# Kernel tuning notes

Hardware: AMD Instinct MI355X
Metric: run time of the kernel (lower is better)

## Reference

```python
import jax, jax.numpy as jnp
import numpy as np

HID = 2048
NH = 16
HD = HID // NH
FF = 8192
SEQ = 2048
B = 1
EPS = 1e-05
ROPE_BASE = 10000.0


def _layernorm(x, w, b):
    mu = jnp.mean(x, axis=-1, keepdims=True)
    var = jnp.mean(jnp.square(x - mu), axis=-1, keepdims=True)
    return (x - mu) * jax.lax.rsqrt(var + EPS) * w + b


def _rope(x, offset):
    # x: [B, S, H, D]; rotate-half LLaMA-style rotary embedding
    S, D = x.shape[1], x.shape[3]
    inv_freq = 1.0 / (ROPE_BASE ** (jnp.arange(0, D, 2, dtype=jnp.float32) / D))  # [D/2]
    pos = jnp.arange(S, dtype=jnp.float32) + offset
    ang = pos[:, None] * inv_freq[None, :]                     # [S, D/2]
    cos = jnp.cos(ang)[None, :, None, :]                       # [1,S,1,D/2]
    sin = jnp.sin(ang)[None, :, None, :]
    x1, x2 = x[..., : D // 2], x[..., D // 2 :]
    return jnp.concatenate([x1 * cos - x2 * sin, x2 * cos + x1 * sin], axis=-1)


def setup_inputs() -> dict:
    key = jax.random.key(0)
    ks = jax.random.split(key, 16)
    sd = 0.02
    inp = {
        "hidden_states": jax.random.normal(ks[0], (B, SEQ, HID), dtype=jnp.float32),
        # additive causal mask as fed to multi_head_attention_forward
        "attention_mask": jnp.where(
            jnp.tril(jnp.ones((SEQ, SEQ), dtype=bool)), 0.0, -1e9
        ).astype(jnp.float32),
        "ln1_w": jnp.ones((HID,), jnp.float32),
        "ln1_b": jnp.zeros((HID,), jnp.float32),
        "ln2_w": jnp.ones((HID,), jnp.float32),
        "ln2_b": jnp.zeros((HID,), jnp.float32),
        "wq": jax.random.normal(ks[1], (HID, HID), jnp.float32) * sd,
        "bq": jnp.zeros((HID,), jnp.float32),
        "wk": jax.random.normal(ks[2], (HID, HID), jnp.float32) * sd,
        "bk": jnp.zeros((HID,), jnp.float32),
        "wv": jax.random.normal(ks[3], (HID, HID), jnp.float32) * sd,
        "bv": jnp.zeros((HID,), jnp.float32),
        "wo": jax.random.normal(ks[4], (HID, HID), jnp.float32) * sd,
        "bo": jnp.zeros((HID,), jnp.float32),
        "w_gate": jax.random.normal(ks[5], (FF, HID), jnp.float32) * sd,
        "w_up": jax.random.normal(ks[6], (FF, HID), jnp.float32) * sd,
        "w_down": jax.random.normal(ks[7], (HID, FF), jnp.float32) * sd,
        "total_seq_len": SEQ,
    }
    return inp


def reference(hidden_states, attention_mask, ln1_w, ln1_b, ln2_w, ln2_b,
              wq, bq, wk, bk, wv, bv, wo, bo, w_gate, w_up, w_down,
              total_seq_len):
    Bv, S, _ = hidden_states.shape
    x = _layernorm(hidden_states, ln1_w, ln1_b)
    q = (x @ wq.T + bq).reshape(Bv, S, NH, HD)
    k = (x @ wk.T + bk).reshape(Bv, S, NH, HD)
    v = (x @ wv.T + bv).reshape(Bv, S, NH, HD)
    offset = total_seq_len - S  # 0 for prefill
    q = _rope(q, offset)
    k = _rope(k, offset)
    # cache of max_sequence_length zeros concatenated with k/v then sliced to the
    # last total_seq_len entries == just the current k/v when total_seq_len == S
    scale = 1.0 / np.sqrt(HD)
    scores = jnp.einsum("bshd,bthd->bhst", q, k) * scale + attention_mask[None, None]
    probs = jax.nn.softmax(scores, axis=-1)
    attn = jnp.einsum("bhst,bthd->bshd", probs, v).reshape(Bv, S, HID)
    attn = attn @ wo.T + bo
    h = hidden_states + attn
    y = _layernorm(h, ln2_w, ln2_b)
    ffn = (jax.nn.silu(y @ w_gate.T) * (y @ w_up.T)) @ w_down.T
    return h + ffn
```

## Files before the change

kernel.cpp:

```cpp
#include <hip/hip_runtime.h>

#define HIDN 2048
#define NHEAD 16
#define HDIM 128
#define FFDIM 8192
#define SEQLEN 2048

typedef __attribute__((ext_vector_type(8))) __bf16 bf16x8;
typedef __attribute__((ext_vector_type(4))) float f32x4;
typedef __attribute__((ext_vector_type(4))) unsigned short u16x4;
typedef __attribute__((ext_vector_type(8))) unsigned short u16x8;

__device__ __forceinline__ unsigned short f2bfu(float f) {
    unsigned int u = __float_as_uint(f);
    unsigned int r = u + 0x7fffu + ((u >> 16) & 1u);
    return (unsigned short)(r >> 16);
}
__device__ __forceinline__ float bfu2f(unsigned short u) {
    return __uint_as_float(((unsigned int)u) << 16);
}

__device__ __forceinline__ void gload16(const void* g, void* l) {
    __builtin_amdgcn_global_load_lds(
        (const __attribute__((address_space(1))) unsigned int*)g,
        (__attribute__((address_space(3))) unsigned int*)l,
        16, 0, 0);
}

__device__ __forceinline__ void conv_groups(const float* __restrict__ src,
                                            unsigned short* __restrict__ dst,
                                            int i0, int stride, int n8) {
    for (int i = i0; i < n8; i += stride) {
        float4 a = ((const float4*)src)[i * 2];
        float4 b = ((const float4*)src)[i * 2 + 1];
        u16x8 v;
        v[0] = f2bfu(a.x); v[1] = f2bfu(a.y); v[2] = f2bfu(a.z); v[3] = f2bfu(a.w);
        v[4] = f2bfu(b.x); v[5] = f2bfu(b.y); v[6] = f2bfu(b.z); v[7] = f2bfu(b.w);
        *(u16x8*)(dst + (size_t)i * 8) = v;
    }
}

__global__ __launch_bounds__(256)
void conv_f32_bf16(const float* __restrict__ src, unsigned short* __restrict__ dst) {
    int i = blockIdx.x * 256 + threadIdx.x;
    conv_groups(src, dst, i, 1 << 30, i + 1);
}

__global__ __launch_bounds__(256)
void conv3_f32_bf16(const float* __restrict__ s0, const float* __restrict__ s1,
                    const float* __restrict__ s2, unsigned short* __restrict__ dst) {
    int i = blockIdx.x * 256 + threadIdx.x;
    int m = i >> 19;
    int li = i & ((1 << 19) - 1);
    const float* s = (m == 0) ? s0 : (m == 1) ? s1 : s2;
    float4 a = ((const float4*)s)[li * 2];
    float4 b = ((const float4*)s)[li * 2 + 1];
    u16x8 v;
    v[0] = f2bfu(a.x); v[1] = f2bfu(a.y); v[2] = f2bfu(a.z); v[3] = f2bfu(a.w);
    v[4] = f2bfu(b.x); v[5] = f2bfu(b.y); v[6] = f2bfu(b.z); v[7] = f2bfu(b.w);
    *(u16x8*)(dst + (size_t)i * 8) = v;
}

__global__ __launch_bounds__(256)
void ln_bf16(const float* __restrict__ x, const float* __restrict__ w,
             const float* __restrict__ b, unsigned short* __restrict__ out) {
    const int row = blockIdx.x;
    const int tid = threadIdx.x;
    const float* xr = x + (size_t)row * HIDN;
    float4 v0 = ((const float4*)xr)[tid];
    float4 v1 = ((const float4*)xr)[tid + 256];
    float s = v0.x + v0.y + v0.z + v0.w + v1.x + v1.y + v1.z + v1.w;
    float q = v0.x*v0.x + v0.y*v0.y + v0.z*v0.z + v0.w*v0.w
            + v1.x*v1.x + v1.y*v1.y + v1.z*v1.z + v1.w*v1.w;
    for (int o = 32; o > 0; o >>= 1) {
        s += __shfl_down(s, o, 64);
        q += __shfl_down(q, o, 64);
    }
    __shared__ float red[8];
    const int wid = tid >> 6;
    if ((tid & 63) == 0) { red[wid] = s; red[4 + wid] = q; }
    __syncthreads();
    float st = red[0] + red[1] + red[2] + red[3];
    float qt = red[4] + red[5] + red[6] + red[7];
    float mu = st * (1.0f / HIDN);
    float var = qt * (1.0f / HIDN) - mu * mu;
    float rs = rsqrtf(var + 1e-5f);
    unsigned short* orow = out + (size_t)row * HIDN;
    int i0 = tid * 4, i1 = (tid + 256) * 4;
    orow[i0 + 0] = f2bfu((v0.x - mu) * rs * w[i0 + 0] + b[i0 + 0]);
    orow[i0 + 1] = f2bfu((v0.y - mu) * rs * w[i0 + 1] + b[i0 + 1]);
    orow[i0 + 2] = f2bfu((v0.z - mu) * rs * w[i0 + 2] + b[i0 + 2]);
    orow[i0 + 3] = f2bfu((v0.w - mu) * rs * w[i0 + 3] + b[i0 + 3]);
    orow[i1 + 0] = f2bfu((v1.x - mu) * rs * w[i1 + 0] + b[i1 + 0]);
    orow[i1 + 1] = f2bfu((v1.y - mu) * rs * w[i1 + 1] + b[i1 + 1]);
    orow[i1 + 2] = f2bfu((v1.z - mu) * rs * w[i1 + 2] + b[i1 + 2]);
    orow[i1 + 3] = f2bfu((v1.w - mu) * rs * w[i1 + 3] + b[i1 + 3]);
}

__global__ __launch_bounds__(256)
void wo_ln(const unsigned short* __restrict__ part, const float* __restrict__ h,
           const float* __restrict__ bo, const float* __restrict__ w,
           const float* __restrict__ b, float* __restrict__ out,
           unsigned short* __restrict__ ybf) {
    const int row = blockIdx.x;
    const int tid = threadIdx.x;
    const int c0 = tid * 4, c1 = (tid + 256) * 4;
    float4 o0 = ((const float4*)(h + (size_t)row * HIDN))[tid];
    float4 o1 = ((const float4*)(h + (size_t)row * HIDN))[tid + 256];
    o0.x += bo[c0]; o0.y += bo[c0 + 1]; o0.z += bo[c0 + 2]; o0.w += bo[c0 + 3];
    o1.x += bo[c1]; o1.y += bo[c1 + 1]; o1.z += bo[c1 + 2]; o1.w += bo[c1 + 3];
#pragma unroll
    for (int sk = 0; sk < 4; ++sk) {
        const unsigned short* pr = part + (size_t)sk * 4194304 + (size_t)row * HIDN;
        u16x4 p0 = *(const u16x4*)(pr + c0);
        u16x4 p1 = *(const u16x4*)(pr + c1);
        o0.x += bfu2f(p0[0]); o0.y += bfu2f(p0[1]); o0.z += bfu2f(p0[2]); o0.w += bfu2f(p0[3]);
        o1.x += bfu2f(p1[0]); o1.y += bfu2f(p1[1]); o1.z += bfu2f(p1[2]); o1.w += bfu2f(p1[3]);
    }
    ((float4*)(out + (size_t)row * HIDN))[tid] = o0;
    ((float4*)(out + (size_t)row * HIDN))[tid + 256] = o1;
    float s = o0.x + o0.y + o0.z + o0.w + o1.x + o1.y + o1.z + o1.w;
    float q = o0.x*o0.x + o0.y*o0.y + o0.z*o0.z + o0.w*o0.w
            + o1.x*o1.x + o1.y*o1.y + o1.z*o1.z + o1.w*o1.w;
    for (int o = 32; o > 0; o >>= 1) {
        s += __shfl_down(s, o, 64);
        q += __shfl_down(q, o, 64);
    }
    __shared__ float red[8];
    const int wid = tid >> 6;
    if ((tid & 63) == 0) { red[wid] = s; red[4 + wid] = q; }
    __syncthreads();
    float st = red[0] + red[1] + red[2] + red[3];
    float qt = red[4] + red[5] + red[6] + red[7];
    float mu = st * (1.0f / HIDN);
    float var = qt * (1.0f / HIDN) - mu * mu;
    float rs = rsqrtf(var + 1e-5f);
    unsigned short* yr = ybf + (size_t)row * HIDN;
    yr[c0 + 0] = f2bfu((o0.x - mu) * rs * w[c0 + 0] + b[c0 + 0]);
    yr[c0 + 1] = f2bfu((o0.y - mu) * rs * w[c0 + 1] + b[c0 + 1]);
    yr[c0 + 2] = f2bfu((o0.z - mu) * rs * w[c0 + 2] + b[c0 + 2]);
    yr[c0 + 3] = f2bfu((o0.w - mu) * rs * w[c0 + 3] + b[c0 + 3]);
    yr[c1 + 0] = f2bfu((o1.x - mu) * rs * w[c1 + 0] + b[c1 + 0]);
    yr[c1 + 1] = f2bfu((o1.y - mu) * rs * w[c1 + 1] + b[c1 + 1]);
    yr[c1 + 2] = f2bfu((o1.z - mu) * rs * w[c1 + 2] + b[c1 + 2]);
    yr[c1 + 3] = f2bfu((o1.w - mu) * rs * w[c1 + 3] + b[c1 + 3]);
}

__global__ __launch_bounds__(256)
void rope_kernel(unsigned short* __restrict__ qk, const int* __restrict__ tsl) {
    int id = blockIdx.x * 256 + threadIdx.x;
    int p  = id & 63;
    int hh = (id >> 6) & 31;
    int s  = id >> 11;
    int off = tsl[0] - SEQLEN;
    float inv = exp2f((float)p * -0.20762050593f);
    float ang = (float)(s + off) * inv;
    float c, sn;
    __sincosf(ang, &sn, &c);
    size_t base = (size_t)s * 4096 + hh * 128 + p;
    float x1 = bfu2f(qk[base]);
    float x2 = bfu2f(qk[base + 64]);
    qk[base]      = f2bfu(x1 * c - x2 * sn);
    qk[base + 64] = f2bfu(x2 * c + x1 * sn);
}

#define BAR __builtin_amdgcn_s_barrier()
#define VM4 asm volatile("s_waitcnt vmcnt(4)" ::: "memory")
#define VM0 asm volatile("s_waitcnt vmcnt(0)" ::: "memory")

#define STAGE_A(tile, h) { const int k0_ = k_start + (tile) * 64;                      \
  _Pragma("unroll") for (int i_ = 0; i_ < 2; ++i_) {                                   \
    int d_ = (h) * 16384 + i_ * 8192 + tid * 16;                                       \
    int r_ = d_ >> 7;                                                                  \
    int cb_ = (d_ & 127) ^ ((r_ & 7) << 4);                                            \
    gload16((const char*)Ab + ((size_t)(brow + r_) * lda + k0_) * 2 + cb_,             \
            smem + ((tile) & 1) * 65536 + (h) * 16384 + i_ * 8192 + w * 1024); } }

#define STAGE_B(tile, h) { const int k0_ = k_start + (tile) * 64;                      \
  _Pragma("unroll") for (int i_ = 0; i_ < 2; ++i_) {                                   \
    int d_ = (h) * 16384 + i_ * 8192 + tid * 16;                                       \
    int r_ = d_ >> 7;                                                                  \
    int cb_ = (d_ & 127) ^ ((r_ & 7) << 4);                                            \
    gload16((const char*)Bb + ((size_t)(bcol + r_) * ldb + k0_) * 2 + cb_,             \
            smem + ((tile) & 1) * 65536 + 32768 + (h) * 16384 + i_ * 8192 + w * 1024); } }

#define LDB(BO)                                                                        \
  _Pragma("unroll") for (int n_ = 0; n_ < 4; ++n_)                                     \
  _Pragma("unroll") for (int kk_ = 0; kk_ < 2; ++kk_)                                  \
    bF[n_][kk_] = *(const bf16x8*)(smem + (BO) + bbase + n_ * 2048 + colb[kk_]);

#define LDA2(BO, MP)                                                                   \
  _Pragma("unroll") for (int dm_ = 0; dm_ < 2; ++dm_)                                  \
  _Pragma("unroll") for (int kk_ = 0; kk_ < 2; ++kk_)                                  \
    aF[dm_][kk_] = *(const bf16x8*)(smem + (BO) + abase + ((MP) * 2 + dm_) * 2048 + colb[kk_]);

#define MM(MP)                                                                         \
  __builtin_amdgcn_s_setprio(1);                                                       \
  _Pragma("unroll") for (int dm_ = 0; dm_ < 2; ++dm_)                                  \
  _Pragma("unroll") for (int n_ = 0; n_ < 4; ++n_)                                     \
  _Pragma("unroll") for (int kk_ = 0; kk_ < 2; ++kk_)                                  \
    acc[(MP) * 2 + dm_][n_] = __builtin_amdgcn_mfma_f32_16x16x32_bf16(                 \
        aF[dm_][kk_], bF[n_][kk_], acc[(MP) * 2 + dm_][n_], 0, 0, 0);                  \
  __builtin_amdgcn_s_setprio(0);

template<int EPI>
__global__ __launch_bounds__(512, 1)
void gemm256(const unsigned short* __restrict__ Ab, int lda,
             const unsigned short* __restrict__ Bb, int ldb,
             int k_len, int nbx, int ldc,
             const float* __restrict__ bias0, const float* __restrict__ bias1,
             const float* __restrict__ bias2,
             unsigned short* __restrict__ outB, unsigned short* __restrict__ outV,
             int ngemm, const float* __restrict__ csrc,
             unsigned short* __restrict__ cdst, int conv_n8) {
    extern __shared__ char smem[];
    const int tid = threadIdx.x;

    if ((int)blockIdx.x >= ngemm) {
        if (blockIdx.y == 0) {
            const int nconv = gridDim.x - ngemm;
            conv_groups(csrc, cdst, (blockIdx.x - ngemm) * 512 + tid, nconv * 512, conv_n8);
        }
        return;
    }

    const int w = tid >> 6, lane = tid & 63;
    const int lr = lane & 15, lg = lane >> 4;
    const int wrow = (w >> 2) * 128;
    const int wc = w & 3;

    const int cpx = nbx >> 3;
    const int xcd = blockIdx.x & 7;
    const int loc = blockIdx.x >> 3;
    const int bx = xcd * cpx + loc % cpx;
    const int by = loc / cpx;
    const int brow = by * 256, bcol = bx * 256;
    const int k_start = blockIdx.y * k_len;

    const int xorv = (lr & 7) << 4;
    int colb[2];
    colb[0] = (lg * 16) ^ xorv;
    colb[1] = (64 + lg * 16) ^ xorv;
    const int abase = (wrow + lr) * 128;
    const int bbase = 32768 + (wc * 64 + lr) * 128;

    f32x4 acc[8][4];
#pragma unroll
    for (int m = 0; m < 8; ++m)
#pragma unroll
        for (int n = 0; n < 4; ++n) acc[m][n] = (f32x4){0.f, 0.f, 0.f, 0.f};

    bf16x8 bF[4][2], aF[2][2];

    const int NT = k_len >> 6;
    const int NIT = NT >> 1;

    STAGE_A(0, 0); STAGE_A(0, 1); STAGE_B(0, 0); STAGE_B(0, 1);
    STAGE_B(1, 0); STAGE_B(1, 1);
    VM4; BAR;

    for (int it = 0; it < NIT; ++it) {
        const int T = 2 * it;
        const bool s2 = (T + 2) < NT, s3 = (T + 3) < NT;
        LDB(0); LDA2(0, 0); STAGE_A(T + 1, 0); MM(0); BAR;
        LDA2(0, 1); STAGE_A(T + 1, 1); MM(1); BAR;
        LDA2(0, 2); if (s2) STAGE_B(T + 2, 0); MM(2); BAR;
        LDA2(0, 3); if (s2) STAGE_B(T + 2, 1); MM(3);
        if (s2) { VM4; } else { VM0; }
        BAR;
        LDB(65536); LDA2(65536, 0); if (s2) STAGE_A(T + 2, 0); MM(0); BAR;
        LDA2(65536, 1); if (s2) STAGE_A(T + 2, 1); MM(1); BAR;
        LDA2(65536, 2); if (s3) STAGE_B(T + 3, 0); MM(2); BAR;
        LDA2(65536, 3); if (s3) STAGE_B(T + 3, 1); MM(3);
        if (s3) { VM4; } else { VM0; }
        BAR;
    }

    char* sw = smem + w * 16384;
    const bool vblk = (EPI == 0) && (bcol >= 4096);

    if (!vblk) {
#pragma unroll
        for (int n = 0; n < 4; ++n) {
            const int col = bcol + wc * 64 + n * 16 + lr;
            float bv = 0.f;
            if (EPI == 0) bv = (col < 2048) ? bias0[col] : bias1[col - 2048];
#pragma unroll
            for (int m = 0; m < 8; ++m)
#pragma unroll
                for (int j = 0; j < 4; ++j) {
                    const int r = m * 16 + lg * 4 + j;
                    const int cb = ((n * 16 + lr) * 2) ^ ((r & 7) << 4);
                    *(unsigned short*)(sw + r * 128 + cb) = f2bfu(acc[m][n][j] + bv);
                }
        }
        const int rl = lane >> 3, cl = lane & 7;
#pragma unroll
        for (int it2 = 0; it2 < 16; ++it2) {
            const int r = it2 * 8 + rl;
            const int cb = (cl * 16) ^ ((r & 7) << 4);
            u16x8 val = *(const u16x8*)(sw + r * 128 + cb);
            const int gr = brow + wrow + r;
            const int gcol = bcol + wc * 64 + cl * 8;
            if (EPI == 0) {
                *(u16x8*)(outB + (size_t)gr * 4096 + gcol) = val;
            } else if (EPI == 1) {
                *(u16x8*)(outB + (size_t)gr * ldc + gcol) = val;
            } else if (EPI == 3) {
                unsigned short* gp = outB + (size_t)gr * ldc + gcol;
                u16x8 gv = *(const u16x8*)gp;
                u16x8 ov;
#pragma unroll
                for (int e = 0; e < 8; ++e) {
                    float g = bfu2f(gv[e]);
                    float uu = bfu2f(val[e]);
                    ov[e] = f2bfu(g / (1.0f + __expf(-g)) * uu);
                }
                *(u16x8*)gp = ov;
            } else {
                *(u16x8*)(outB + (size_t)blockIdx.y * 4194304 + (size_t)gr * ldc + gcol) = val;
            }
        }
    } else {
#pragma unroll
        for (int n = 0; n < 4; ++n) {
            const int c = n * 16 + lr;
            const float bv = bias2[bcol - 4096 + wc * 64 + c];
            const int cx = (c & 7) << 4;
#pragma unroll
            for (int m = 0; m < 8; ++m) {
                const int r0 = m * 16 + lg * 4;
                u16x4 pk;
#pragma unroll
                for (int j = 0; j < 4; ++j) pk[j] = f2bfu(acc[m][n][j] + bv);
                *(u16x4*)(sw + c * 256 + ((r0 * 2) ^ cx)) = pk;
            }
        }
        const int cg = lane >> 4, rl2 = lane & 15;
#pragma unroll
        for (int it2 = 0; it2 < 16; ++it2) {
            const int c = it2 * 4 + cg;
            const int rb = (rl2 * 16) ^ ((c & 7) << 4);
            u16x8 val = *(const u16x8*)(sw + c * 256 + rb);
            const int d = bcol - 4096 + wc * 64 + c;
            *(u16x8*)(outV + (size_t)d * SEQLEN + brow + wrow + rl2 * 8) = val;
        }
    }
}

__global__ __launch_bounds__(256)
void reduce4_add(const unsigned short* __restrict__ part, float* __restrict__ out) {
    int i = blockIdx.x * 256 + threadIdx.x;
    float4 o = ((const float4*)out)[i];
#pragma unroll
    for (int sk = 0; sk < 4; ++sk) {
        u16x4 p = ((const u16x4*)(part + (size_t)sk * 4194304))[i];
        o.x += bfu2f(p[0]); o.y += bfu2f(p[1]); o.z += bfu2f(p[2]); o.w += bfu2f(p[3]);
    }
    ((float4*)out)[i] = o;
}

#define PST 72
__global__ __launch_bounds__(256)
void attn_kernel(const unsigned short* __restrict__ QK, const unsigned short* __restrict__ VT,
                 unsigned short* __restrict__ O,
                 const float* __restrict__ csrc, unsigned short* __restrict__ cdst,
                 int conv_n8) {
    __shared__ __align__(16) unsigned short Ks[2][64 * 128];
    __shared__ __align__(16) unsigned short Vs[2][128 * 64];
    __shared__ __align__(16) unsigned short Ps[4][16 * PST];
    const int tid = threadIdx.x;

    if ((int)blockIdx.x >= 256) {
        const int nconv = gridDim.x - 256;
        conv_groups(csrc, cdst, (blockIdx.x - 256) * 256 + tid, nconv * 256, conv_n8);
        return;
    }

    const int lane = tid & 63;
    const int w = tid >> 6;
    const int lr = lane & 15, lg = lane >> 4;

    const int id = blockIdx.x;
    const int h = ((id & 7) << 1) | ((id >> 3) & 1);
    const int p = id >> 4;

    const unsigned short* Kb = QK + 2048 + h * 128;
    const unsigned short* Vb = VT + (size_t)(h * 128) * SEQLEN;

    int krow[4], kcb[4], vrow[4], vcb[4];
#pragma unroll
    for (int ch = 0; ch < 4; ++ch) {
        int d = ch * 4096 + w * 1024 + lane * 16;
        krow[ch] = d >> 8;
        kcb[ch]  = (d & 255) ^ ((krow[ch] & 7) << 4);
        vrow[ch] = d >> 7;
        vcb[ch]  = (d & 127) ^ ((vrow[ch] & 7) << 4);
    }

    const float sc = 0.08838834764831845f;

#pragma unroll 1
    for (int seg = 0; seg < 2; ++seg) {
        const int qb = seg ? (31 - p) : p;
        const int qw = qb * 64 + w * 16;
        const unsigned short* Qb = QK + (size_t)qw * 4096 + h * 128;

        bf16x8 qa[4];
#pragma unroll
        for (int c = 0; c < 4; ++c)
            qa[c] = *(const bf16x8*)(Qb + (size_t)lr * 4096 + c * 32 + lg * 8);

        f32x4 acc[8];
#pragma unroll
        for (int dt = 0; dt < 8; ++dt) acc[dt] = (f32x4){0.f, 0.f, 0.f, 0.f};
        float mrow[4] = {-INFINITY, -INFINITY, -INFINITY, -INFINITY};
        float lrow[4] = {0.f, 0.f, 0.f, 0.f};
        const int ntile = qb + 1;

#pragma unroll
        for (int ch = 0; ch < 4; ++ch) {
            gload16(Kb + (size_t)krow[ch] * 4096 + (kcb[ch] >> 1),
                    (char*)&Ks[0][0] + ch * 4096 + w * 1024);
            gload16(Vb + (size_t)vrow[ch] * SEQLEN + (vcb[ch] >> 1),
                    (char*)&Vs[0][0] + ch * 4096 + w * 1024);
        }
        __syncthreads();

        for (int tt = 0; tt < ntile; ++tt) {
            const int cur = tt & 1;
            const int t0 = tt * 64;
            if (tt + 1 < ntile) {
                const int t1 = t0 + 64;
#pragma unroll
                for (int ch = 0; ch < 4; ++ch) {
                    gload16(Kb + (size_t)(t1 + krow[ch]) * 4096 + (kcb[ch] >> 1),
                            (char*)&Ks[cur ^ 1][0] + ch * 4096 + w * 1024);
                    gload16(Vb + (size_t)vrow[ch] * SEQLEN + t1 + (vcb[ch] >> 1),
                            (char*)&Vs[cur ^ 1][0] + ch * 4096 + w * 1024);
                }
            }
            f32x4 s[4];
#pragma unroll
            for (int th = 0; th < 4; ++th) s[th] = (f32x4){0.f, 0.f, 0.f, 0.f};
            __builtin_amdgcn_s_setprio(1);
#pragma unroll
            for (int th = 0; th < 4; ++th) {
                const int row = th * 16 + lr;
#pragma unroll
                for (int c = 0; c < 4; ++c) {
                    bf16x8 kb = *(const bf16x8*)((char*)&Ks[cur][0] + row * 256 +
                                                 ((c * 64 + lg * 16) ^ ((lr & 7) << 4)));
                    s[th] = __builtin_amdgcn_mfma_f32_16x16x32_bf16(qa[c], kb, s[th], 0, 0, 0);
                }
            }
            __builtin_amdgcn_s_setprio(0);
#pragma unroll
            for (int th = 0; th < 4; ++th) {
                int tg = t0 + th * 16 + lr;
#pragma unroll
                for (int jj = 0; jj < 4; ++jj) {
                    int qg = qw + lg * 4 + jj;
                    s[th][jj] = s[th][jj] * sc + (tg <= qg ? 0.f : -1e9f);
                }
            }
            float mt[4];
#pragma unroll
            for (int jj = 0; jj < 4; ++jj)
                mt[jj] = fmaxf(fmaxf(s[0][jj], s[1][jj]), fmaxf(s[2][jj], s[3][jj]));
#pragma unroll
            for (int o = 8; o > 0; o >>= 1)
#pragma unroll
                for (int jj = 0; jj < 4; ++jj) mt[jj] = fmaxf(mt[jj], __shfl_xor(mt[jj], o, 16));
            bool need = false;
#pragma unroll
            for (int jj = 0; jj < 4; ++jj) need = need || (mt[jj] > mrow[jj] + 4.0f);
            if (__any(need)) {
#pragma unroll
                for (int jj = 0; jj < 4; ++jj) {
                    float mn = fmaxf(mrow[jj], mt[jj]);
                    float a = __expf(mrow[jj] - mn);
                    mrow[jj] = mn;
                    lrow[jj] *= a;
#pragma unroll
                    for (int dt = 0; dt < 8; ++dt) acc[dt][jj] *= a;
                }
            }
            float ps[4] = {0.f, 0.f, 0.f, 0.f};
#pragma unroll
            for (int th = 0; th < 4; ++th)
#pragma unroll
                for (int jj = 0; jj < 4; ++jj) {
                    float pp = __expf(s[th][jj] - mrow[jj]);
                    s[th][jj] = pp;
                    ps[jj] += pp;
                }
#pragma unroll
            for (int o = 8; o > 0; o >>= 1)
#pragma unroll
                for (int jj = 0; jj < 4; ++jj) ps[jj] += __shfl_xor(ps[jj], o, 16);
#pragma unroll
            for (int jj = 0; jj < 4; ++jj) lrow[jj] += ps[jj];
#pragma unroll
            for (int th = 0; th < 4; ++th)
#pragma unroll
                for (int jj = 0; jj < 4; ++jj)
                    Ps[w][(lg * 4 + jj) * PST + th * 16 + lr] = f2bfu(s[th][jj]);
            bf16x8 pa[2];
#pragma unroll
            for (int ks = 0; ks < 2; ++ks)
                pa[ks] = *(const bf16x8*)&Ps[w][lr * PST + ks * 32 + lg * 8];
            __builtin_amdgcn_s_setprio(1);
#pragma unroll
            for (int dt = 0; dt < 8; ++dt) {
                const int d = dt * 16 + lr;
#pragma unroll
                for (int ks = 0; ks < 2; ++ks) {
                    bf16x8 vb = *(const bf16x8*)((char*)&Vs[cur][0] + d * 128 +
                                                 ((ks * 64 + lg * 16) ^ ((lr & 7) << 4)));
                    acc[dt] = __builtin_amdgcn_mfma_f32_16x16x32_bf16(pa[ks], vb, acc[dt], 0, 0, 0);
                }
            }
            __builtin_amdgcn_s_setprio(0);
            __syncthreads();
        }
        float invl[4];
#pragma unroll
        for (int jj = 0; jj < 4; ++jj) invl[jj] = 1.0f / lrow[jj];
#pragma unroll
        for (int dt = 0; dt < 8; ++dt)
#pragma unroll
            for (int jj = 0; jj < 4; ++jj)
                O[(size_t)(qw + lg * 4 + jj) * HIDN + h * HDIM + dt * 16 + lr] =
                    f2bfu(acc[dt][jj] * invl[jj]);
    }
}

extern "C" void kernel_launch(void* const* d_in, const int* in_sizes, int n_in,
                              void* d_out, int out_size, void* d_ws, size_t ws_size,
                              hipStream_t stream) {
    const float* hidden = (const float*)d_in[0];
    const float* ln1w = (const float*)d_in[2];
    const float* ln1b = (const float*)d_in[3];
    const float* ln2w = (const float*)d_in[4];
    const float* ln2b = (const float*)d_in[5];
    const float* wq = (const float*)d_in[6];
    const float* bq = (const float*)d_in[7];
    const float* wk = (const float*)d_in[8];
    const float* bk = (const float*)d_in[9];
    const float* wv = (const float*)d_in[10];
    const float* bv = (const float*)d_in[11];
    const float* wo = (const float*)d_in[12];
    const float* bo = (const float*)d_in[13];
    const float* wg = (const float*)d_in[14];
    const float* wu = (const float*)d_in[15];
    const float* wd = (const float*)d_in[16];
    const int* tsl = (const int*)d_in[17];
    float* out = (float*)d_out;

    char* ws = (char*)d_ws;
    const size_t MB = 1024 * 1024;
    unsigned short* Wbuf = (unsigned short*)(ws);
    unsigned short* qk   = (unsigned short*)(ws + 32 * MB);
    unsigned short* vt   = (unsigned short*)(ws + 48 * MB);
    unsigned short* x_bf = (unsigned short*)(ws + 56 * MB);
    unsigned short* g_bf = (unsigned short*)(ws + 64 * MB);
    unsigned short* part = qk;
    unsigned short* y_bf = vt;

    const int HID2 = HIDN * HIDN;
    const int CONV_HID = HID2 / 8 / 256;
    const int CONV_FF  = FFDIM * HIDN / 8 / 256;
    const size_t LDSZ = 131072;

    const bool big_ws = ws_size >= 128 * MB;
    unsigned short* wgBuf = big_ws ? (unsigned short*)(ws + 96 * MB) : Wbuf;

    conv3_f32_bf16<<<3 * CONV_HID, 256, 0, stream>>>(wq, wk, wv, Wbuf);
    ln_bf16<<<SEQLEN, 256, 0, stream>>>(hidden, ln1w, ln1b, x_bf);
    gemm256<0><<<dim3(192 + 64, 1), 512, LDSZ, stream>>>(
        x_bf, HIDN, Wbuf, HIDN, HIDN, 24, 0, bq, bk, bv, qk, vt,
        192, wo, Wbuf + 3 * (size_t)HID2, HID2 / 8);
    rope_kernel<<<SEQLEN * 32 * 64 / 256, 256, 0, stream>>>(qk, tsl);

    if (big_ws) {
        attn_kernel<<<512, 256, 0, stream>>>(qk, vt, x_bf, wg, wgBuf, FFDIM * HIDN / 8);
    } else {
        attn_kernel<<<256, 256, 0, stream>>>(qk, vt, x_bf, nullptr, nullptr, 0);
    }

    gemm256<4><<<dim3(64, 4), 512, LDSZ, stream>>>(
        x_bf, HIDN, Wbuf + 3 * (size_t)HID2, HIDN, 512, 8, HIDN,
        nullptr, nullptr, nullptr, g_bf, nullptr, 64, nullptr, nullptr, 0);
    wo_ln<<<SEQLEN, 256, 0, stream>>>(g_bf, hidden, bo, ln2w, ln2b, out, y_bf);

    if (!big_ws)
        conv_f32_bf16<<<CONV_FF, 256, 0, stream>>>(wg, Wbuf);
    gemm256<1><<<dim3(256, 1), 512, LDSZ, stream>>>(
        y_bf, HIDN, wgBuf, HIDN, HIDN, 32, FFDIM,
        nullptr, nullptr, nullptr, g_bf, nullptr, 256, nullptr, nullptr, 0);
    conv_f32_bf16<<<CONV_FF, 256, 0, stream>>>(wu, Wbuf);
    gemm256<3><<<dim3(256, 1), 512, LDSZ, stream>>>(
        y_bf, HIDN, Wbuf, HIDN, HIDN, 32, FFDIM,
        nullptr, nullptr, nullptr, g_bf, nullptr, 256, nullptr, nullptr, 0);
    conv_f32_bf16<<<CONV_FF, 256, 0, stream>>>(wd, Wbuf);
    gemm256<4><<<dim3(64, 4), 512, LDSZ, stream>>>(
        g_bf, FFDIM, Wbuf, FFDIM, 2048, 8, HIDN,
        nullptr, nullptr, nullptr, part, nullptr, 64, nullptr, nullptr, 0);
    reduce4_add<<<4096, 256, 0, stream>>>(part, out);
}
```

Measured before the change: 430.2 us.

## Overlap all three FFN weight conversions with attention and use exp2 softmax

When the workspace is large enough, the extra blocks launched alongside the attention kernel now convert the gate, up and down FFN weights (not only the gate) into separate bf16 buffers. This removes the standalone conversion launches between the FFN GEMMs and hides that work behind attention. The softmax also folds log2(e) into the score scale and uses exp2f instead of __expf, saving a multiply per exponent. The cost is more workspace use and more conversion work competing with attention blocks, and the path depends on ws_size thresholds.

Result: faster. 413.8 us (-3.8%).

```diff
diff --git a/kernel.cpp b/kernel.cpp
--- a/kernel.cpp
+++ b/kernel.cpp
@@ -33,6 +33,26 @@
     for (int i = i0; i < n8; i += stride) {
         float4 a = ((const float4*)src)[i * 2];
         float4 b = ((const float4*)src)[i * 2 + 1];
+        u16x8 v;
+        v[0] = f2bfu(a.x); v[1] = f2bfu(a.y); v[2] = f2bfu(a.z); v[3] = f2bfu(a.w);
+        v[4] = f2bfu(b.x); v[5] = f2bfu(b.y); v[6] = f2bfu(b.z); v[7] = f2bfu(b.w);
+        *(u16x8*)(dst + (size_t)i * 8) = v;
+    }
+}
+
+__device__ __forceinline__ void conv_tail3(const float* __restrict__ s0,
+                                           const float* __restrict__ s1,
+                                           const float* __restrict__ s2,
+                                           unsigned short* __restrict__ dst,
+                                           int i0, int stride, int nmat) {
+    const int FF8 = FFDIM * HIDN / 8;
+    const int tot = nmat * FF8;
+    for (int i = i0; i < tot; i += stride) {
+        int m = i >> 21;
+        int li = i & (FF8 - 1);
+        const float* s = (m == 0) ? s0 : (m == 1) ? s1 : s2;
+        float4 a = ((const float4*)s)[li * 2];
+        float4 b = ((const float4*)s)[li * 2 + 1];
         u16x8 v;
         v[0] = f2bfu(a.x); v[1] = f2bfu(a.y); v[2] = f2bfu(a.z); v[3] = f2bfu(a.w);
         v[4] = f2bfu(b.x); v[5] = f2bfu(b.y); v[6] = f2bfu(b.z); v[7] = f2bfu(b.w);
@@ -364,8 +384,9 @@
 __global__ __launch_bounds__(256)
 void attn_kernel(const unsigned short* __restrict__ QK, const unsigned short* __restrict__ VT,
                  unsigned short* __restrict__ O,
-                 const float* __restrict__ csrc, unsigned short* __restrict__ cdst,
-                 int conv_n8) {
+                 const float* __restrict__ c0, const float* __restrict__ c1,
+                 const float* __restrict__ c2, unsigned short* __restrict__ cdst,
+                 int nmat) {
     __shared__ __align__(16) unsigned short Ks[2][64 * 128];
     __shared__ __align__(16) unsigned short Vs[2][128 * 64];
     __shared__ __align__(16) unsigned short Ps[4][16 * PST];
@@ -373,7 +394,7 @@
 
     if ((int)blockIdx.x >= 256) {
         const int nconv = gridDim.x - 256;
-        conv_groups(csrc, cdst, (blockIdx.x - 256) * 256 + tid, nconv * 256, conv_n8);
+        conv_tail3(c0, c1, c2, cdst, (blockIdx.x - 256) * 256 + tid, nconv * 256, nmat);
         return;
     }
 
@@ -398,7 +419,7 @@
         vcb[ch]  = (d & 127) ^ ((vrow[ch] & 7) << 4);
     }
 
-    const float sc = 0.08838834764831845f;
+    const float sc2 = 0.08838834764831845f * 1.44269504089f;
 
 #pragma unroll 1
     for (int seg = 0; seg < 2; ++seg) {
@@ -461,7 +482,7 @@
 #pragma unroll
                 for (int jj = 0; jj < 4; ++jj) {
                     int qg = qw + lg * 4 + jj;
-                    s[th][jj] = s[th][jj] * sc + (tg <= qg ? 0.f : -1e9f);
+                    s[th][jj] = s[th][jj] * sc2 + (tg <= qg ? 0.f : -1e9f);
                 }
             }
             float mt[4];
@@ -479,7 +500,7 @@
 #pragma unroll
                 for (int jj = 0; jj < 4; ++jj) {
                     float mn = fmaxf(mrow[jj], mt[jj]);
-                    float a = __expf(mrow[jj] - mn);
+                    float a = exp2f(mrow[jj] - mn);
                     mrow[jj] = mn;
                     lrow[jj] *= a;
 #pragma unroll
@@ -491,7 +512,7 @@
             for (int th = 0; th < 4; ++th)
 #pragma unroll
                 for (int jj = 0; jj < 4; ++jj) {
-                    float pp = __expf(s[th][jj] - mrow[jj]);
+                    float pp = exp2f(s[th][jj] - mrow[jj]);
                     s[th][jj] = pp;
                     ps[jj] += pp;
                 }
@@ -569,12 +590,18 @@
     unsigned short* y_bf = vt;
 
     const int HID2 = HIDN * HIDN;
+    const int FFE  = FFDIM * HIDN;
     const int CONV_HID = HID2 / 8 / 256;
-    const int CONV_FF  = FFDIM * HIDN / 8 / 256;
+    const int CONV_FF  = FFE / 8 / 256;
     const size_t LDSZ = 131072;
 
-    const bool big_ws = ws_size >= 128 * MB;
-    unsigned short* wgBuf = big_ws ? (unsigned short*)(ws + 96 * MB) : Wbuf;
+    int nmat = 0;
+    if (ws_size >= 192 * MB) nmat = 3;
+    else if (ws_size >= 160 * MB) nmat = 2;
+    else if (ws_size >= 128 * MB) nmat = 1;
+    unsigned short* wgBuf = (nmat > 0) ? (unsigned short*)(ws + 96 * MB) : Wbuf;
+    unsigned short* wuBuf = (nmat > 1) ? wgBuf + (size_t)FFE : Wbuf;
+    unsigned short* wdBuf = (nmat > 2) ? wgBuf + 2 * (size_t)FFE : Wbuf;
 
     conv3_f32_bf16<<<3 * CONV_HID, 256, 0, stream>>>(wq, wk, wv, Wbuf);
     ln_bf16<<<SEQLEN, 256, 0, stream>>>(hidden, ln1w, ln1b, x_bf);
@@ -583,10 +610,11 @@
         192, wo, Wbuf + 3 * (size_t)HID2, HID2 / 8);
     rope_kernel<<<SEQLEN * 32 * 64 / 256, 256, 0, stream>>>(qk, tsl);
 
-    if (big_ws) {
-        attn_kernel<<<512, 256, 0, stream>>>(qk, vt, x_bf, wg, wgBuf, FFDIM * HIDN / 8);
+    if (nmat > 0) {
+        attn_kernel<<<512, 256, 0, stream>>>(qk, vt, x_bf, wg, wu, wd, wgBuf, nmat);
     } else {
-        attn_kernel<<<256, 256, 0, stream>>>(qk, vt, x_bf, nullptr, nullptr, 0);
+        attn_kernel<<<256, 256, 0, stream>>>(qk, vt, x_bf, nullptr, nullptr, nullptr,
+                                             nullptr, 0);
     }
 
     gemm256<4><<<dim3(64, 4), 512, LDSZ, stream>>>(
@@ -594,18 +622,17 @@
         nullptr, nullptr, nullptr, g_bf, nullptr, 64, nullptr, nullptr, 0);
     wo_ln<<<SEQLEN, 256, 0, stream>>>(g_bf, hidden, bo, ln2w, ln2b, out, y_bf);
 
-    if (!big_ws)
-        conv_f32_bf16<<<CONV_FF, 256, 0, stream>>>(wg, Wbuf);
+    if (nmat < 1) conv_f32_bf16<<<CONV_FF, 256, 0, stream>>>(wg, Wbuf);
     gemm256<1><<<dim3(256, 1), 512, LDSZ, stream>>>(
         y_bf, HIDN, wgBuf, HIDN, HIDN, 32, FFDIM,
         nullptr, nullptr, nullptr, g_bf, nullptr, 256, nullptr, nullptr, 0);
-    conv_f32_bf16<<<CONV_FF, 256, 0, stream>>>(wu, Wbuf);
+    if (nmat < 2) conv_f32_bf16<<<CONV_FF, 256, 0, stream>>>(wu, Wbuf);
     gemm256<3><<<dim3(256, 1), 512, LDSZ, stream>>>(
-        y_bf, HIDN, Wbuf, HIDN, HIDN, 32, FFDIM,
+        y_bf, HIDN, wuBuf, HIDN, HIDN, 32, FFDIM,
         nullptr, nullptr, nullptr, g_bf, nullptr, 256, nullptr, nullptr, 0);
-    conv_f32_bf16<<<CONV_FF, 256, 0, stream>>>(wd, Wbuf);
+    if (nmat < 3) conv_f32_bf16<<<CONV_FF, 256, 0, stream>>>(wd, Wbuf);
     gemm256<4><<<dim3(64, 4), 512, LDSZ, stream>>>(
-        g_bf, FFDIM, Wbuf, FFDIM, 2048, 8, HIDN,
+        g_bf, FFDIM, wdBuf, FFDIM, 2048, 8, HIDN,
         nullptr, nullptr, nullptr, part, nullptr, 64, nullptr, nullptr, 0);
     reduce4_add<<<4096, 256, 0, stream>>>(part, out);
 }
```
